# Kernel optimization log

Measured on AMD Instinct MI355X. Metric: run time of the kernel, lower is better.

Reference implementation:

```python
import jax, jax.numpy as jnp
import numpy as np

B, N, H, L = 4096, 512, 1024, 8


def setup_inputs() -> dict:
    key = jax.random.key(0)
    k1, k2, k3, k4 = jax.random.split(key, 4)
    x = jax.random.normal(k1, (B, N), dtype=jnp.float32)
    beta = jax.random.uniform(k2, (H, L, N), dtype=jnp.float32)  # torch.rand init
    bound = 1.0 / np.sqrt(N)
    W = jax.random.uniform(k3, (H, N), minval=-bound, maxval=bound, dtype=jnp.float32)
    b = jax.random.uniform(k4, (H,), minval=-bound, maxval=bound, dtype=jnp.float32)
    return {"x": x, "beta": beta, "W": W, "b": b}


def reference(x, beta, W, b):
    # Original computes c[h,j,k] = sum_l beta[h,l,j]*beta[h,l,k], then
    # out_fm[b,h] = sum_{j<k} x[b,j]*x[b,k]*c[h,j,k]  (strict upper-tri mask).
    # FM identity: sum_{j<k} x_j x_k <v_j, v_k>
    #            = 0.5 * sum_l [ (sum_j x_j v_{lj})^2 - sum_j x_j^2 v_{lj}^2 ]
    s = jnp.einsum('bn,hln->bhl', x, beta)            # (B, H, L)
    ssq = jnp.einsum('bn,hln->bhl', x * x, beta * beta)  # (B, H, L)
    fm = 0.5 * jnp.sum(s * s - ssq, axis=-1)          # (B, H)
    linear_out = x @ W.T + b                          # (B, H)
    return fm + linear_out
```

## Files before the change

### kernel.cpp

```cpp
#include <hip/hip_runtime.h>
#include <stdint.h>

static constexpr int B_DIM = 4096;
static constexpr int N_DIM = 512;
static constexpr int H_DIM = 1024;
static constexpr int L_DIM = 8;
static constexpr int HL    = H_DIM * L_DIM;
static constexpr int KC    = 2 * N_DIM;

typedef __attribute__((ext_vector_type(8))) short short8;
typedef __attribute__((ext_vector_type(8))) unsigned short u16x8;
typedef __attribute__((ext_vector_type(4))) float f32x4;

__device__ __forceinline__ uint16_t f2bf(float f) {
  uint32_t u = __float_as_uint(f);
  u += 0x7fffu + ((u >> 16) & 1u);
  return (uint16_t)(u >> 16);
}

__device__ __forceinline__ void stage16(const uint16_t* g, uint16_t* l) {
  __builtin_amdgcn_global_load_lds(
      (const __attribute__((address_space(1))) void*)g,
      (__attribute__((address_space(3))) void*)l, 16, 0, 0);
}

static constexpr int PREP_T0 = HL * N_DIM / 8;
static constexpr int PREP_T1 = B_DIM * N_DIM / 8;
static constexpr int PREP_T2 = H_DIM * N_DIM / 8;

__global__ void prep_kernel(const float* __restrict__ x, const float* __restrict__ beta,
                            const float* __restrict__ W,
                            uint16_t* __restrict__ xcomb, uint16_t* __restrict__ betab,
                            uint16_t* __restrict__ combW) {
  int t = blockIdx.x * 256 + threadIdx.x;
  if (t < PREP_T0) {
    const f32x4* src = (const f32x4*)(beta + (size_t)t * 8);
    f32x4 a = src[0], b = src[1];
    u16x8 o;
#pragma unroll
    for (int i = 0; i < 4; ++i) { o[i] = f2bf(a[i]); o[4 + i] = f2bf(b[i]); }
    *(u16x8*)(betab + (size_t)t * 8) = o;
    return;
  }
  t -= PREP_T0;
  if (t < PREP_T1) {
    int bb = t >> 6, n8 = (t & 63) * 8;
    const f32x4* src = (const f32x4*)(x + (size_t)bb * N_DIM + n8);
    f32x4 a = src[0], b = src[1];
    u16x8 lo, hi;
#pragma unroll
    for (int i = 0; i < 4; ++i) {
      lo[i] = f2bf(a[i]);        lo[4 + i] = f2bf(b[i]);
      hi[i] = f2bf(a[i] * a[i]); hi[4 + i] = f2bf(b[i] * b[i]);
    }
    *(u16x8*)(xcomb + (size_t)bb * KC + n8)         = lo;
    *(u16x8*)(xcomb + (size_t)bb * KC + N_DIM + n8) = hi;
    return;
  }
  t -= PREP_T1;
  int h = t >> 6, n8 = (t & 63) * 8;
  const f32x4* wsrc = (const f32x4*)(W + (size_t)h * N_DIM + n8);
  f32x4 wa = wsrc[0], wb = wsrc[1];
  u16x8 lo;
#pragma unroll
  for (int i = 0; i < 4; ++i) { lo[i] = f2bf(wa[i]); lo[4 + i] = f2bf(wb[i]); }
  *(u16x8*)(combW + (size_t)h * KC + n8) = lo;
  float s[8] = {};
#pragma unroll
  for (int l = 0; l < L_DIM; ++l) {
    const f32x4* bsrc = (const f32x4*)(beta + ((size_t)h * L_DIM + l) * N_DIM + n8);
    f32x4 a = bsrc[0], b = bsrc[1];
#pragma unroll
    for (int i = 0; i < 4; ++i) { s[i] += a[i] * a[i]; s[4 + i] += b[i] * b[i]; }
  }
  u16x8 hi;
#pragma unroll
  for (int i = 0; i < 8; ++i) hi[i] = f2bf(-0.5f * s[i]);
  *(u16x8*)(combW + (size_t)h * KC + N_DIM + n8) = hi;
}

__global__ __launch_bounds__(256) void fm_kernel(
    const uint16_t* __restrict__ xcomb,
    const uint16_t* __restrict__ betab,
    const uint16_t* __restrict__ combW,
    const float* __restrict__ bias,
    float* __restrict__ out)
{
  __shared__ __align__(16) uint16_t As[128 * 128];
  __shared__ __align__(16) uint16_t Bs[128 * 64];
  __shared__ __align__(16) uint16_t Ws[16 * 128];

  const int tid  = threadIdx.x;
  const int lane = tid & 63;
  const int wave = tid >> 6;
  const int wm = wave >> 1, wn = wave & 1;
  const int fr   = lane & 15;
  const int quad = lane >> 4;
  const int row0  = blockIdx.y * 128;
  const int col0  = blockIdx.x * 128;
  const int hcol0 = blockIdx.x * 16;

  f32x4 acc[4][4] = {};
  f32x4 lacc[4]   = {};

  for (int kt = 0; kt < N_DIM; kt += 64) {
#pragma unroll
    for (int u = 0; u < 8; ++u) {
      int s = tid + u * 256, m = s >> 4, cp = s & 15, c = cp ^ (m & 15);
      int col = (c >> 3) * N_DIM + kt + (c & 7) * 8;
      stage16(xcomb + (size_t)(row0 + m) * KC + col, As + s * 8);
    }
#pragma unroll
    for (int u = 0; u < 4; ++u) {
      int s = tid + u * 256, m = s >> 3, cp = s & 7, c = cp ^ (m & 7);
      stage16(betab + (size_t)(col0 + m) * N_DIM + kt + c * 8, Bs + s * 8);
    }
    {
      int m = tid >> 4, cp = tid & 15, c = cp ^ m;
      int col = (c >> 3) * N_DIM + kt + (c & 7) * 8;
      stage16(combW + (size_t)(hcol0 + m) * KC + col, Ws + tid * 8);
    }
    __syncthreads();

#pragma unroll
    for (int kk2 = 0; kk2 < 2; ++kk2) {
      const int cbase = kk2 * 4 + quad;
      short8 af[4], bf[4], al[4], wf;
#pragma unroll
      for (int i = 0; i < 4; ++i) {
        int m = wm * 64 + i * 16 + fr;
        af[i] = *(const short8*)(As + (m * 16 + (cbase ^ (m & 15))) * 8);
      }
#pragma unroll
      for (int j = 0; j < 4; ++j) {
        int m = wn * 64 + j * 16 + fr;
        bf[j] = *(const short8*)(Bs + (m * 8 + (cbase ^ (m & 7))) * 8);
      }
      wf = *(const short8*)(Ws + (fr * 16 + ((wn * 8 + cbase) ^ fr)) * 8);
      if (wn == 0) {
#pragma unroll
        for (int i = 0; i < 4; ++i) al[i] = af[i];
      } else {
#pragma unroll
        for (int i = 0; i < 4; ++i) {
          int m = wm * 64 + i * 16 + fr;
          al[i] = *(const short8*)(As + (m * 16 + ((8 + cbase) ^ (m & 15))) * 8);
        }
      }
#pragma unroll
      for (int i = 0; i < 4; ++i)
#pragma unroll
        for (int j = 0; j < 4; ++j)
          acc[i][j] = __builtin_amdgcn_mfma_f32_16x16x32_bf16(af[i], bf[j], acc[i][j], 0, 0, 0);
#pragma unroll
      for (int i = 0; i < 4; ++i)
        lacc[i] = __builtin_amdgcn_mfma_f32_16x16x32_bf16(al[i], wf, lacc[i], 0, 0, 0);
    }
    __syncthreads();
  }

  float* red = (float*)As;
  if (wn == 0) {
#pragma unroll
    for (int i = 0; i < 4; ++i)
#pragma unroll
      for (int r = 0; r < 4; ++r)
        red[(wm * 64 + i * 16 + quad * 4 + r) * 16 + fr] = lacc[i][r];
  }
  __syncthreads();
  if (wn == 1) {
#pragma unroll
    for (int i = 0; i < 4; ++i)
#pragma unroll
      for (int r = 0; r < 4; ++r)
        red[(wm * 64 + i * 16 + quad * 4 + r) * 16 + fr] += lacc[i][r];
  }
  __syncthreads();
#pragma unroll
  for (int i = 0; i < 4; ++i)
#pragma unroll
    for (int j = 0; j < 4; ++j) {
      const int hin = wn * 8 + j * 2 + (fr >> 3);
#pragma unroll
      for (int r = 0; r < 4; ++r) {
        float v = acc[i][j][r];
        v = v * v;
        v += __shfl_xor(v, 1);
        v += __shfl_xor(v, 2);
        v += __shfl_xor(v, 4);
        if ((lane & 7) == 0)
          red[(wm * 64 + i * 16 + quad * 4 + r) * 16 + hin] += 0.5f * v;
      }
    }
  __syncthreads();
#pragma unroll
  for (int e = tid; e < 2048; e += 256) {
    int r = e >> 4, hc = e & 15;
    out[(size_t)(row0 + r) * H_DIM + hcol0 + hc] = red[e] + bias[hcol0 + hc];
  }
}

extern "C" void kernel_launch(void* const* d_in, const int* in_sizes, int n_in,
                              void* d_out, int out_size, void* d_ws, size_t ws_size,
                              hipStream_t stream) {
  const float* x    = (const float*)d_in[0];
  const float* beta = (const float*)d_in[1];
  const float* W    = (const float*)d_in[2];
  const float* bias = (const float*)d_in[3];
  float* out = (float*)d_out;

  uint16_t* xcomb = (uint16_t*)d_ws;
  uint16_t* betab = xcomb + (size_t)B_DIM * KC;
  uint16_t* combW = betab + (size_t)HL * N_DIM;

  const int prep_threads = PREP_T0 + PREP_T1 + PREP_T2;
  prep_kernel<<<prep_threads / 256, 256, 0, stream>>>(x, beta, W, xcomb, betab, combW);

  fm_kernel<<<dim3(HL / 128, B_DIM / 128), 256, 0, stream>>>(
      xcomb, betab, combW, bias, out);
}
```

Before: 165.0 us.

## Fuse prep and GEMM into persistent cooperative kernel; square x in-register

Merges the bf16 conversion pass and the FM GEMM into a single cooperative persistent kernel of 512 blocks that runs a grid-wide sync between phases and then loops over four output tiles per block. The x-squared half of the combined input is no longer stored; it is computed on the fly from the bf16 x fragments inside the linear-term MFMA path. This halves the A-tile staging and the workspace for x. The change also pads the reduction buffer stride and vectorizes the output store. It adds grid-sync cost, depends on cooperative launch being supported (with a two-kernel fallback), and squaring a bf16 value changes rounding slightly compared with squaring the fp32 value.

```diff
diff --git a/kernel.cpp b/kernel.cpp
--- a/kernel.cpp
+++ b/kernel.cpp
@@ -1,12 +1,14 @@
 #include <hip/hip_runtime.h>
+#include <hip/hip_cooperative_groups.h>
 #include <stdint.h>
+
+namespace cg = cooperative_groups;
 
 static constexpr int B_DIM = 4096;
 static constexpr int N_DIM = 512;
 static constexpr int H_DIM = 1024;
 static constexpr int L_DIM = 8;
 static constexpr int HL    = H_DIM * L_DIM;
-static constexpr int KC    = 2 * N_DIM;
 
 typedef __attribute__((ext_vector_type(8))) short short8;
 typedef __attribute__((ext_vector_type(8))) unsigned short u16x8;
@@ -24,91 +26,81 @@
       (__attribute__((address_space(3))) void*)l, 16, 0, 0);
 }
 
-static constexpr int PREP_T0 = HL * N_DIM / 8;
-static constexpr int PREP_T1 = B_DIM * N_DIM / 8;
-static constexpr int PREP_T2 = H_DIM * N_DIM / 8;
-
-__global__ void prep_kernel(const float* __restrict__ x, const float* __restrict__ beta,
-                            const float* __restrict__ W,
-                            uint16_t* __restrict__ xcomb, uint16_t* __restrict__ betab,
-                            uint16_t* __restrict__ combW) {
-  int t = blockIdx.x * 256 + threadIdx.x;
-  if (t < PREP_T0) {
+__device__ __forceinline__ short8 sq8(short8 a) {
+  union { short8 s; uint32_t u[4]; } in, out;
+  in.s = a;
+#pragma unroll
+  for (int d = 0; d < 4; ++d) {
+    uint32_t lo = in.u[d] << 16;
+    uint32_t hi = in.u[d] & 0xffff0000u;
+    float fl = __uint_as_float(lo), fh = __uint_as_float(hi);
+    fl *= fl; fh *= fh;
+    out.u[d] = (__float_as_uint(fh) & 0xffff0000u) | (__float_as_uint(fl) >> 16);
+  }
+  return out.s;
+}
+
+__device__ __forceinline__ void prep_phase(int gtid, int gsize,
+    const float* __restrict__ x, const float* __restrict__ beta,
+    const float* __restrict__ W, uint16_t* __restrict__ xb,
+    uint16_t* __restrict__ betab, uint16_t* __restrict__ combW) {
+  for (int t = gtid; t < HL * N_DIM / 8; t += gsize) {
     const f32x4* src = (const f32x4*)(beta + (size_t)t * 8);
     f32x4 a = src[0], b = src[1];
     u16x8 o;
 #pragma unroll
     for (int i = 0; i < 4; ++i) { o[i] = f2bf(a[i]); o[4 + i] = f2bf(b[i]); }
     *(u16x8*)(betab + (size_t)t * 8) = o;
-    return;
-  }
-  t -= PREP_T0;
-  if (t < PREP_T1) {
-    int bb = t >> 6, n8 = (t & 63) * 8;
-    const f32x4* src = (const f32x4*)(x + (size_t)bb * N_DIM + n8);
+  }
+  for (int t = gtid; t < B_DIM * N_DIM / 8; t += gsize) {
+    const f32x4* src = (const f32x4*)(x + (size_t)t * 8);
     f32x4 a = src[0], b = src[1];
-    u16x8 lo, hi;
-#pragma unroll
-    for (int i = 0; i < 4; ++i) {
-      lo[i] = f2bf(a[i]);        lo[4 + i] = f2bf(b[i]);
-      hi[i] = f2bf(a[i] * a[i]); hi[4 + i] = f2bf(b[i] * b[i]);
-    }
-    *(u16x8*)(xcomb + (size_t)bb * KC + n8)         = lo;
-    *(u16x8*)(xcomb + (size_t)bb * KC + N_DIM + n8) = hi;
-    return;
-  }
-  t -= PREP_T1;
-  int h = t >> 6, n8 = (t & 63) * 8;
-  const f32x4* wsrc = (const f32x4*)(W + (size_t)h * N_DIM + n8);
-  f32x4 wa = wsrc[0], wb = wsrc[1];
-  u16x8 lo;
-#pragma unroll
-  for (int i = 0; i < 4; ++i) { lo[i] = f2bf(wa[i]); lo[4 + i] = f2bf(wb[i]); }
-  *(u16x8*)(combW + (size_t)h * KC + n8) = lo;
-  float s[8] = {};
-#pragma unroll
-  for (int l = 0; l < L_DIM; ++l) {
-    const f32x4* bsrc = (const f32x4*)(beta + ((size_t)h * L_DIM + l) * N_DIM + n8);
-    f32x4 a = bsrc[0], b = bsrc[1];
-#pragma unroll
-    for (int i = 0; i < 4; ++i) { s[i] += a[i] * a[i]; s[4 + i] += b[i] * b[i]; }
-  }
-  u16x8 hi;
-#pragma unroll
-  for (int i = 0; i < 8; ++i) hi[i] = f2bf(-0.5f * s[i]);
-  *(u16x8*)(combW + (size_t)h * KC + N_DIM + n8) = hi;
-}
-
-__global__ __launch_bounds__(256) void fm_kernel(
-    const uint16_t* __restrict__ xcomb,
-    const uint16_t* __restrict__ betab,
-    const uint16_t* __restrict__ combW,
-    const float* __restrict__ bias,
-    float* __restrict__ out)
-{
-  __shared__ __align__(16) uint16_t As[128 * 128];
-  __shared__ __align__(16) uint16_t Bs[128 * 64];
-  __shared__ __align__(16) uint16_t Ws[16 * 128];
-
-  const int tid  = threadIdx.x;
+    u16x8 o;
+#pragma unroll
+    for (int i = 0; i < 4; ++i) { o[i] = f2bf(a[i]); o[4 + i] = f2bf(b[i]); }
+    *(u16x8*)(xb + (size_t)t * 8) = o;
+  }
+  for (int t = gtid; t < H_DIM * N_DIM / 8; t += gsize) {
+    int h = t >> 6, n8 = (t & 63) * 8;
+    const f32x4* wsrc = (const f32x4*)(W + (size_t)h * N_DIM + n8);
+    f32x4 wa = wsrc[0], wb = wsrc[1];
+    u16x8 lo;
+#pragma unroll
+    for (int i = 0; i < 4; ++i) { lo[i] = f2bf(wa[i]); lo[4 + i] = f2bf(wb[i]); }
+    *(u16x8*)(combW + (size_t)h * 1024 + n8) = lo;
+    float s[8] = {};
+#pragma unroll
+    for (int l = 0; l < L_DIM; ++l) {
+      const f32x4* bsrc = (const f32x4*)(beta + ((size_t)h * L_DIM + l) * N_DIM + n8);
+      f32x4 a = bsrc[0], b = bsrc[1];
+#pragma unroll
+      for (int i = 0; i < 4; ++i) { s[i] += a[i] * a[i]; s[4 + i] += b[i] * b[i]; }
+    }
+    u16x8 hi;
+#pragma unroll
+    for (int i = 0; i < 8; ++i) hi[i] = f2bf(-0.5f * s[i]);
+    *(u16x8*)(combW + (size_t)h * 1024 + 512 + n8) = hi;
+  }
+}
+
+__device__ __forceinline__ void gemm_tile(int bx, int by, int tid,
+    const uint16_t* __restrict__ xb, const uint16_t* __restrict__ betab,
+    const uint16_t* __restrict__ combW, const float* __restrict__ bias,
+    float* __restrict__ out, uint16_t* As, uint16_t* Bs, uint16_t* Ws) {
   const int lane = tid & 63;
   const int wave = tid >> 6;
   const int wm = wave >> 1, wn = wave & 1;
-  const int fr   = lane & 15;
-  const int quad = lane >> 4;
-  const int row0  = blockIdx.y * 128;
-  const int col0  = blockIdx.x * 128;
-  const int hcol0 = blockIdx.x * 16;
+  const int fr = lane & 15, quad = lane >> 4;
+  const int row0 = by * 128, col0 = bx * 128, hcol0 = bx * 16;
 
   f32x4 acc[4][4] = {};
-  f32x4 lacc[4]   = {};
+  f32x4 lacc[4] = {};
 
   for (int kt = 0; kt < N_DIM; kt += 64) {
 #pragma unroll
-    for (int u = 0; u < 8; ++u) {
-      int s = tid + u * 256, m = s >> 4, cp = s & 15, c = cp ^ (m & 15);
-      int col = (c >> 3) * N_DIM + kt + (c & 7) * 8;
-      stage16(xcomb + (size_t)(row0 + m) * KC + col, As + s * 8);
+    for (int u = 0; u < 4; ++u) {
+      int s = tid + u * 256, m = s >> 3, cp = s & 7, c = cp ^ (m & 7);
+      stage16(xb + (size_t)(row0 + m) * N_DIM + kt + c * 8, As + s * 8);
     }
 #pragma unroll
     for (int u = 0; u < 4; ++u) {
@@ -118,18 +110,18 @@
     {
       int m = tid >> 4, cp = tid & 15, c = cp ^ m;
       int col = (c >> 3) * N_DIM + kt + (c & 7) * 8;
-      stage16(combW + (size_t)(hcol0 + m) * KC + col, Ws + tid * 8);
+      stage16(combW + (size_t)(hcol0 + m) * 1024 + col, Ws + tid * 8);
     }
     __syncthreads();
 
 #pragma unroll
     for (int kk2 = 0; kk2 < 2; ++kk2) {
       const int cbase = kk2 * 4 + quad;
-      short8 af[4], bf[4], al[4], wf;
+      short8 af[4], bf[4], wf;
 #pragma unroll
       for (int i = 0; i < 4; ++i) {
         int m = wm * 64 + i * 16 + fr;
-        af[i] = *(const short8*)(As + (m * 16 + (cbase ^ (m & 15))) * 8);
+        af[i] = *(const short8*)(As + (m * 8 + (cbase ^ (m & 7))) * 8);
       }
 #pragma unroll
       for (int j = 0; j < 4; ++j) {
@@ -137,24 +129,20 @@
         bf[j] = *(const short8*)(Bs + (m * 8 + (cbase ^ (m & 7))) * 8);
       }
       wf = *(const short8*)(Ws + (fr * 16 + ((wn * 8 + cbase) ^ fr)) * 8);
-      if (wn == 0) {
-#pragma unroll
-        for (int i = 0; i < 4; ++i) al[i] = af[i];
-      } else {
-#pragma unroll
-        for (int i = 0; i < 4; ++i) {
-          int m = wm * 64 + i * 16 + fr;
-          al[i] = *(const short8*)(As + (m * 16 + ((8 + cbase) ^ (m & 15))) * 8);
-        }
-      }
 #pragma unroll
       for (int i = 0; i < 4; ++i)
 #pragma unroll
         for (int j = 0; j < 4; ++j)
           acc[i][j] = __builtin_amdgcn_mfma_f32_16x16x32_bf16(af[i], bf[j], acc[i][j], 0, 0, 0);
-#pragma unroll
-      for (int i = 0; i < 4; ++i)
-        lacc[i] = __builtin_amdgcn_mfma_f32_16x16x32_bf16(al[i], wf, lacc[i], 0, 0, 0);
+      if (wn == 0) {
+#pragma unroll
+        for (int i = 0; i < 4; ++i)
+          lacc[i] = __builtin_amdgcn_mfma_f32_16x16x32_bf16(af[i], wf, lacc[i], 0, 0, 0);
+      } else {
+#pragma unroll
+        for (int i = 0; i < 4; ++i)
+          lacc[i] = __builtin_amdgcn_mfma_f32_16x16x32_bf16(sq8(af[i]), wf, lacc[i], 0, 0, 0);
+      }
     }
     __syncthreads();
   }
@@ -165,7 +153,7 @@
     for (int i = 0; i < 4; ++i)
 #pragma unroll
       for (int r = 0; r < 4; ++r)
-        red[(wm * 64 + i * 16 + quad * 4 + r) * 16 + fr] = lacc[i][r];
+        red[(wm * 64 + i * 16 + quad * 4 + r) * 20 + fr] = lacc[i][r];
   }
   __syncthreads();
   if (wn == 1) {
@@ -173,7 +161,7 @@
     for (int i = 0; i < 4; ++i)
 #pragma unroll
       for (int r = 0; r < 4; ++r)
-        red[(wm * 64 + i * 16 + quad * 4 + r) * 16 + fr] += lacc[i][r];
+        red[(wm * 64 + i * 16 + quad * 4 + r) * 20 + fr] += lacc[i][r];
   }
   __syncthreads();
 #pragma unroll
@@ -189,15 +177,53 @@
         v += __shfl_xor(v, 2);
         v += __shfl_xor(v, 4);
         if ((lane & 7) == 0)
-          red[(wm * 64 + i * 16 + quad * 4 + r) * 16 + hin] += 0.5f * v;
-      }
-    }
-  __syncthreads();
-#pragma unroll
-  for (int e = tid; e < 2048; e += 256) {
-    int r = e >> 4, hc = e & 15;
-    out[(size_t)(row0 + r) * H_DIM + hcol0 + hc] = red[e] + bias[hcol0 + hc];
-  }
+          red[(wm * 64 + i * 16 + quad * 4 + r) * 20 + hin] += 0.5f * v;
+      }
+    }
+  __syncthreads();
+#pragma unroll
+  for (int u = 0; u < 2; ++u) {
+    int s = tid + u * 256;
+    int r = s >> 2, hc4 = (s & 3) * 4;
+    f32x4 b4 = *(const f32x4*)(bias + hcol0 + hc4);
+    f32x4 v  = *(const f32x4*)(red + r * 20 + hc4);
+    f32x4 o;
+#pragma unroll
+    for (int c = 0; c < 4; ++c) o[c] = v[c] + b4[c];
+    *(f32x4*)(out + (size_t)(row0 + r) * H_DIM + hcol0 + hc4) = o;
+  }
+  __syncthreads();
+}
+
+__global__ __launch_bounds__(256, 2) void fused_all(
+    const float* __restrict__ x, const float* __restrict__ beta,
+    const float* __restrict__ W, const float* __restrict__ bias,
+    uint16_t* __restrict__ xb, uint16_t* __restrict__ betab,
+    uint16_t* __restrict__ combW, float* __restrict__ out) {
+  __shared__ __align__(16) uint16_t As[128 * 64];
+  __shared__ __align__(16) uint16_t Bs[128 * 64];
+  __shared__ __align__(16) uint16_t Ws[16 * 128];
+  const int tid = threadIdx.x, bid = blockIdx.x;
+  prep_phase(bid * 256 + tid, 512 * 256, x, beta, W, xb, betab, combW);
+  cg::this_grid().sync();
+#pragma unroll 1
+  for (int tt = 0; tt < 4; ++tt) {
+    int T = tt * 512 + bid;
+    gemm_tile(T & 63, T >> 6, tid, xb, betab, combW, bias, out, As, Bs, Ws);
+  }
+}
+
+__global__ void prep_only(const float* x, const float* beta, const float* W,
+                          uint16_t* xb, uint16_t* betab, uint16_t* combW) {
+  prep_phase(blockIdx.x * 256 + threadIdx.x, gridDim.x * 256, x, beta, W, xb, betab, combW);
+}
+__global__ __launch_bounds__(256) void gemm_only(
+    const uint16_t* xb, const uint16_t* betab, const uint16_t* combW,
+    const float* bias, float* out) {
+  __shared__ __align__(16) uint16_t As[128 * 64];
+  __shared__ __align__(16) uint16_t Bs[128 * 64];
+  __shared__ __align__(16) uint16_t Ws[16 * 128];
+  gemm_tile(blockIdx.x, blockIdx.y, threadIdx.x, xb, betab, combW, bias, out, As, Bs, Ws);
 }
 
 extern "C" void kernel_launch(void* const* d_in, const int* in_sizes, int n_in,
@@ -209,13 +235,16 @@
   const float* bias = (const float*)d_in[3];
   float* out = (float*)d_out;
 
-  uint16_t* xcomb = (uint16_t*)d_ws;
-  uint16_t* betab = xcomb + (size_t)B_DIM * KC;
+  uint16_t* xb    = (uint16_t*)d_ws;
+  uint16_t* betab = xb + (size_t)B_DIM * N_DIM;
   uint16_t* combW = betab + (size_t)HL * N_DIM;
 
-  const int prep_threads = PREP_T0 + PREP_T1 + PREP_T2;
-  prep_kernel<<<prep_threads / 256, 256, 0, stream>>>(x, beta, W, xcomb, betab, combW);
-
-  fm_kernel<<<dim3(HL / 128, B_DIM / 128), 256, 0, stream>>>(
-      xcomb, betab, combW, bias, out);
-}
+  void* args[] = {(void*)&x, (void*)&beta, (void*)&W, (void*)&bias,
+                  (void*)&xb, (void*)&betab, (void*)&combW, (void*)&out};
+  hipError_t e = hipLaunchCooperativeKernel((const void*)fused_all,
+                                            dim3(512), dim3(256), args, 0, stream);
+  if (e != hipSuccess) {
+    prep_only<<<2048, 256, 0, stream>>>(x, beta, W, xb, betab, combW);
+    gemm_only<<<dim3(64, 32), 256, 0, stream>>>(xb, betab, combW, bias, out);
+  }
+}
```

After: 226.8 us. +37.5%, slower.
